# Kernel tuning notes

Hardware: AMD Instinct MI355X
Metric: run time of the kernel (lower is better)

## Reference

```python
import jax, jax.numpy as jnp
import numpy as np

BEAM_SIZE = 16


def setup_inputs() -> dict:
    key = jax.random.key(0)
    ks = jax.random.split(key, 9)
    B, N, S, A, Ai, E = 4, 48, 32, 16, 8, 512
    unaries = jax.random.normal(ks[0], (B, N, S), jnp.float32)
    behaviors = jax.random.normal(ks[1], (B, N, S, A), jnp.float32)
    interactions = jax.random.normal(ks[2], (B, N, N, S, S, Ai), jnp.float32)
    masks = jnp.ones((B, N), jnp.bool_)
    behavior_masks = jax.random.bernoulli(ks[3], 0.5, (S, A))
    interaction_masks = jax.random.bernoulli(ks[4], 0.5, (S, S, Ai))
    binary_edges = jax.random.randint(ks[5], (B, E, 2), 0, N, jnp.int32)
    binary_masks = jnp.ones((B, E), jnp.bool_)
    targets = jax.random.randint(ks[6], (B, N), 0, S, jnp.int32)
    weight_param_unary = jax.random.uniform(ks[7], (S,), jnp.float32)
    weight_param_binary = jax.random.uniform(ks[8], (S, S), jnp.float32)
    return dict(unaries=unaries, behaviors=behaviors, interactions=interactions,
                weight_param_unary=weight_param_unary, weight_param_binary=weight_param_binary,
                masks=masks, behavior_masks=behavior_masks, interaction_masks=interaction_masks,
                binary_edges=binary_edges, binary_masks=binary_masks, targets=targets)


def _forward(unaries, behaviors, interactions, weight_param_unary, weight_param_binary,
             masks, behavior_masks, interaction_masks, binary_edges, binary_masks, targets):
    sg = jax.lax.stop_gradient  # mirrors torch.no_grad blocks
    B, N, S = unaries.shape
    E = binary_edges.shape[1]
    K = min(BEAM_SIZE, S)
    dt = unaries.dtype

    m = masks[..., None].astype(dt)                                  # (B,N,1)
    masked_unaries = sg(unaries * m)                                 # no_grad
    bmask = behavior_masks.astype(dt)                                # (S,A)
    acnt = bmask.sum(-1)
    acnt = jnp.where(acnt == 0, jnp.ones((), dt), acnt)              # (S,)
    behaviors_unaries = sg(((behaviors * bmask).sum(-1) / acnt) * m) # (B,N,S), no_grad

    weighted_unaries = masked_unaries + weight_param_unary * behaviors_unaries

    # --- beam selection (targets forced to beam slot 0 via +inf scatter) ---
    bi = jnp.arange(B)[:, None]
    ni = jnp.arange(N)[None, :]
    _u = weighted_unaries.at[bi, ni, targets].set(jnp.inf)
    beam_targets = jax.lax.top_k(sg(_u), K)[1]                       # (B,N,K) int
    beam_unary = jnp.take_along_axis(weighted_unaries, beam_targets, axis=2)  # (B,N,K)

    # --- binary potentials: masked mean over interaction actions ---
    imask = interaction_masks.astype(dt)                             # (S,S,Ai)
    icnt = imask.sum(-1)
    icnt = jnp.where(icnt == 0, jnp.ones((), dt), icnt)              # (S,S)
    masked_inter = (interactions * imask).sum(-1) / icnt             # (B,N,N,S,S)

    eb = jnp.arange(B)[:, None]
    sel = masked_inter[eb, binary_edges[..., 0], binary_edges[..., 1]]  # (B,E,S,S)
    bt1 = beam_targets[eb, binary_edges[..., 0]]                     # (B,E,K)
    bt2 = beam_targets[eb, binary_edges[..., 1]]                     # (B,E,K)
    bin_phis_init = sg(sel[jnp.arange(B)[:, None, None, None],
                           jnp.arange(E)[None, :, None, None],
                           bt1[:, :, :, None], bt2[:, :, None, :]])  # (B,E,K,K), no_grad
    bin_phis = bin_phis_init * weight_param_binary[bt1[:, :, :, None], bt2[:, :, None, :]]

    # --- piecewise pseudo-likelihood loss ---
    norm_unary = jax.nn.log_softmax(beam_unary, axis=-1)
    gold_unary = jnp.where(masks, norm_unary[:, :, 0], jnp.zeros((), dt))
    pll = gold_unary.sum(-1)                                         # (B,)
    norm_bin = jax.nn.log_softmax(bin_phis.reshape(B, E, K * K), axis=-1).reshape(B, E, K, K)
    gold_bin = jnp.where(binary_masks, norm_bin[:, :, 0, 0], jnp.zeros((), dt))
    pll = pll + gold_bin.sum(-1)
    nll = -(pll / masks.sum(-1).astype(dt)).mean()
    return nll


def reference(unaries, behaviors, interactions, weight_param_unary, weight_param_binary,
              masks, behavior_masks, interaction_masks, binary_edges, binary_masks, targets):
    return _forward(unaries, behaviors, interactions, weight_param_unary, weight_param_binary,
                    masks, behavior_masks, interaction_masks, binary_edges, binary_masks, targets)
```

## Files before the change

### kernel.cpp

```cpp
#include <hip/hip_runtime.h>
#include <hip/hip_bf16.h>
#include <math.h>

#define BB 4
#define NN 48
#define SS 32
#define AA 16
#define AI 8
#define EE 512
#define KK 16
#define NNODE (BB * NN)
#define NEDGE (BB * EE)

#define WS_CBIN  0
#define WS_BEAM  32768
#define WS_NG    45056
#define WS_EG    46080

__device__ __forceinline__ bool read_mask(const void* p, int idx, int flag) {
    if (flag == 1) return ((const unsigned char*)p)[idx] != 0;
    if (flag == 2) return ((const float*)p)[idx] != 0.0f;
    return ((const int*)p)[idx] != 0;
}

__device__ __forceinline__ int detect_flag(const void* bmask, int lane) {
    unsigned int wrd = ((const unsigned int*)bmask)[lane & 31];
    bool anyF = __any(wrd == 0x3F800000u);
    bool anyG = __any(wrd > 1u);
    return anyF ? 2 : (anyG ? 1 : 0);
}

__global__ __launch_bounds__(256) void node_kernel(
    const float* __restrict__ unaries,
    const float* __restrict__ behaviors,
    const float* __restrict__ wpu,
    const float* __restrict__ wpb,
    const void* masks, const void* bmask, const void* imask,
    const int* __restrict__ targets,
    float* __restrict__ cbin,
    int* __restrict__ beam,
    float* __restrict__ node_gold)
{
    int tid = threadIdx.x;
    int wid = tid >> 6, lane = tid & 63;
    int flag = detect_flag(bmask, lane);

    if (blockIdx.x < 48) {
        int node = blockIdx.x * 4 + wid;
        float m = read_mask(masks, node, flag) ? 1.f : 0.f;
        int tgt = targets[node];

        float val = -INFINITY, key = -INFINITY;
        if (lane < SS) {
            int s = lane;
            float u = unaries[node * SS + s];
            const float* bp = behaviors + ((size_t)node * SS + s) * AA;
            float cnt = 0.f, raw = 0.f;
            #pragma unroll
            for (int a = 0; a < AA; ++a) {
                bool mm = read_mask(bmask, s * AA + a, flag);
                cnt += mm ? 1.f : 0.f;
                raw += mm ? bp[a] : 0.f;
            }
            if (cnt == 0.f) cnt = 1.f;
            val = m * (u + wpu[s] * (raw / cnt));
            key = (s == tgt) ? INFINITY : val;
        }

        int rank = 0;
        #pragma unroll
        for (int t = 0; t < SS; ++t) {
            float kt = __shfl(key, t, 64);
            rank += (kt > key) || (kt == key && t < lane);
        }
        bool sel = (lane < SS) && (rank < KK);
        if (sel) beam[node * KK + rank] = lane;

        float mv = sel ? val : -INFINITY;
        #pragma unroll
        for (int off = 32; off >= 1; off >>= 1)
            mv = fmaxf(mv, __shfl_xor(mv, off, 64));
        float se = sel ? expf(val - mv) : 0.f;
        #pragma unroll
        for (int off = 32; off >= 1; off >>= 1)
            se += __shfl_xor(se, off, 64);
        float vt = __shfl(val, tgt, 64);
        if (lane == 0)
            node_gold[node] = (m > 0.f) ? (vt - mv - logf(se)) : 0.f;
    } else {
        int idx = (blockIdx.x - 48) * 256 + tid;
        int p = idx >> 3;
        float cnt = 0.f;
        #pragma unroll
        for (int a = 0; a < AI; ++a)
            cnt += read_mask(imask, p * AI + a, flag) ? 1.f : 0.f;
        if (cnt == 0.f) cnt = 1.f;
        bool mm = read_mask(imask, idx, flag);
        cbin[idx] = mm ? (wpb[p] / cnt) : 0.f;
    }
}

__global__ __launch_bounds__(256) void edge_kernel(
    const float* __restrict__ interactions,
    const int* __restrict__ edges,
    const void* binmask, const void* bmask,
    const float* __restrict__ cbin,
    const int* __restrict__ beam,
    float* __restrict__ edge_gold)
{
    int be = blockIdx.x;
    int b = be >> 9;
    int tid = threadIdx.x;
    int wid = tid >> 6, lane = tid & 63;

    int n1 = edges[be * 2 + 0];
    int n2 = edges[be * 2 + 1];

    int i = tid >> 4, j = tid & 15;
    int s1 = beam[(b * NN + n1) * KK + i];
    int s2 = beam[(b * NN + n2) * KK + j];
    int p = s1 * SS + s2;

    size_t base = (((size_t)(b * NN + n1) * NN + n2) * (SS * SS) + p) * AI;
    float4 x0 = *(const float4*)(interactions + base);
    float4 x1 = *(const float4*)(interactions + base + 4);
    float4 c0 = *(const float4*)(cbin + p * AI);
    float4 c1 = *(const float4*)(cbin + p * AI + 4);
    float phi = x0.x * c0.x + x0.y * c0.y + x0.z * c0.z + x0.w * c0.w
              + x1.x * c1.x + x1.y * c1.y + x1.z * c1.z + x1.w * c1.w;

    __shared__ float sred[4];
    float v = phi;
    #pragma unroll
    for (int off = 32; off >= 1; off >>= 1)
        v = fmaxf(v, __shfl_xor(v, off, 64));
    if (lane == 0) sred[wid] = v;
    __syncthreads();
    float mx = fmaxf(fmaxf(sred[0], sred[1]), fmaxf(sred[2], sred[3]));
    __syncthreads();
    float e = expf(phi - mx);
    #pragma unroll
    for (int off = 32; off >= 1; off >>= 1)
        e += __shfl_xor(e, off, 64);
    if (lane == 0) sred[wid] = e;
    __syncthreads();
    if (tid == 0) {
        int flag = detect_flag(bmask, lane);
        float s = sred[0] + sred[1] + sred[2] + sred[3];
        float gold = phi - mx - logf(s);
        bool bm = read_mask(binmask, be, flag);
        edge_gold[be] = bm ? gold : 0.f;
    }
}

__global__ __launch_bounds__(256) void final_kernel(
    const void* masks, const void* bmask,
    const float* __restrict__ node_gold,
    const float* __restrict__ edge_gold,
    float* __restrict__ out)
{
    int tid = threadIdx.x;
    int b = tid >> 6;
    int lane = tid & 63;
    int flag = detect_flag(bmask, lane);

    float sum = 0.f, cnt = 0.f;
    if (lane < NN) {
        sum += node_gold[b * NN + lane];
        cnt += read_mask(masks, b * NN + lane, flag) ? 1.f : 0.f;
    }
    for (int e = lane; e < EE; e += 64)
        sum += edge_gold[b * EE + e];

    #pragma unroll
    for (int off = 32; off >= 1; off >>= 1) {
        sum += __shfl_xor(sum, off, 64);
        cnt += __shfl_xor(cnt, off, 64);
    }
    __shared__ float sp[4];
    if (lane == 0) sp[b] = sum / cnt;
    __syncthreads();
    if (tid == 0)
        out[0] = -(sp[0] + sp[1] + sp[2] + sp[3]) * (1.f / BB);
}

extern "C" void kernel_launch(void* const* d_in, const int* in_sizes, int n_in,
                              void* d_out, int out_size, void* d_ws, size_t ws_size,
                              hipStream_t stream) {
    const float* unaries      = (const float*)d_in[0];
    const float* behaviors    = (const float*)d_in[1];
    const float* interactions = (const float*)d_in[2];
    const float* wpu          = (const float*)d_in[3];
    const float* wpb          = (const float*)d_in[4];
    const void*  masks        = d_in[5];
    const void*  bmask        = d_in[6];
    const void*  imask        = d_in[7];
    const int*   edges        = (const int*)d_in[8];
    const void*  binmask      = d_in[9];
    const int*   targets      = (const int*)d_in[10];
    float* out = (float*)d_out;

    char* ws = (char*)d_ws;
    float* cbin      = (float*)(ws + WS_CBIN);
    int*   beamp     = (int*)(ws + WS_BEAM);
    float* node_gold = (float*)(ws + WS_NG);
    float* edge_gold = (float*)(ws + WS_EG);

    node_kernel<<<80, 256, 0, stream>>>(unaries, behaviors, wpu, wpb,
                                        masks, bmask, imask, targets,
                                        cbin, beamp, node_gold);
    edge_kernel<<<NEDGE, 256, 0, stream>>>(interactions, edges, binmask, bmask,
                                           cbin, beamp, edge_gold);
    final_kernel<<<1, 256, 0, stream>>>(masks, bmask, node_gold, edge_gold, out);
}
```

Before: 21.64 us.

## Vectorize mask/behavior loads, pack two edges per block, merge softmax reductions

Behavior and mask reads in the node kernel become float4/uint4 vector loads, and the cbin precompute gives each thread one pair with two vector stores, cutting its grid from 80 to 52 blocks. Beam slot assignment now uses a ballot/popcount order with the target in slot 0. The edge kernel handles two edges per 512-thread block and fuses the max and sum-exp reductions into one online-softmax pass with a single barrier. The aim is fewer memory instructions, fewer blocks and fewer syncs, at the cost of more exp calls and a changed beam ordering within slots 1..15.

```diff
diff --git a/kernel.cpp b/kernel.cpp
--- a/kernel.cpp
+++ b/kernel.cpp
@@ -54,14 +54,40 @@
         if (lane < SS) {
             int s = lane;
             float u = unaries[node * SS + s];
-            const float* bp = behaviors + ((size_t)node * SS + s) * AA;
+
+            const float4* bp4 = (const float4*)(behaviors + ((size_t)node * SS + s) * AA);
+            float4 b0 = bp4[0], b1 = bp4[1], b2 = bp4[2], b3 = bp4[3];
+            float bv[16] = {b0.x,b0.y,b0.z,b0.w, b1.x,b1.y,b1.z,b1.w,
+                            b2.x,b2.y,b2.z,b2.w, b3.x,b3.y,b3.z,b3.w};
+
+            float bmv[16];
+            if (flag == 1) {
+                uint4 v = *(const uint4*)((const unsigned char*)bmask + s * 16);
+                unsigned int w4[4] = {v.x, v.y, v.z, v.w};
+                #pragma unroll
+                for (int k = 0; k < 16; ++k)
+                    bmv[k] = ((w4[k >> 2] >> ((k & 3) * 8)) & 255u) ? 1.f : 0.f;
+            } else if (flag == 0) {
+                const uint4* ip = (const uint4*)((const int*)bmask + s * 16);
+                #pragma unroll
+                for (int r = 0; r < 4; ++r) {
+                    uint4 v = ip[r];
+                    bmv[r*4+0] = v.x ? 1.f : 0.f; bmv[r*4+1] = v.y ? 1.f : 0.f;
+                    bmv[r*4+2] = v.z ? 1.f : 0.f; bmv[r*4+3] = v.w ? 1.f : 0.f;
+                }
+            } else {
+                const float4* fp = (const float4*)((const float*)bmask + s * 16);
+                #pragma unroll
+                for (int r = 0; r < 4; ++r) {
+                    float4 v = fp[r];
+                    bmv[r*4+0] = v.x != 0.f ? 1.f : 0.f; bmv[r*4+1] = v.y != 0.f ? 1.f : 0.f;
+                    bmv[r*4+2] = v.z != 0.f ? 1.f : 0.f; bmv[r*4+3] = v.w != 0.f ? 1.f : 0.f;
+                }
+            }
+
             float cnt = 0.f, raw = 0.f;
             #pragma unroll
-            for (int a = 0; a < AA; ++a) {
-                bool mm = read_mask(bmask, s * AA + a, flag);
-                cnt += mm ? 1.f : 0.f;
-                raw += mm ? bp[a] : 0.f;
-            }
+            for (int k = 0; k < 16; ++k) { cnt += bmv[k]; raw += bmv[k] * bv[k]; }
             if (cnt == 0.f) cnt = 1.f;
             val = m * (u + wpu[s] * (raw / cnt));
             key = (s == tgt) ? INFINITY : val;
@@ -74,7 +100,14 @@
             rank += (kt > key) || (kt == key && t < lane);
         }
         bool sel = (lane < SS) && (rank < KK);
-        if (sel) beam[node * KK + rank] = lane;
+
+        bool sel_nt = sel && (lane != tgt);
+        unsigned long long bal = __ballot(sel_nt);
+        if (sel) {
+            int slot = (lane == tgt) ? 0
+                       : 1 + __popcll(bal & ((1ull << lane) - 1ull));
+            beam[node * KK + slot] = lane;
+        }
 
         float mv = sel ? val : -INFINITY;
         #pragma unroll
@@ -88,19 +121,36 @@
         if (lane == 0)
             node_gold[node] = (m > 0.f) ? (vt - mv - logf(se)) : 0.f;
     } else {
-        int idx = (blockIdx.x - 48) * 256 + tid;
-        int p = idx >> 3;
-        float cnt = 0.f;
-        #pragma unroll
-        for (int a = 0; a < AI; ++a)
-            cnt += read_mask(imask, p * AI + a, flag) ? 1.f : 0.f;
+        int p = (blockIdx.x - 48) * 256 + tid;
+        float imv[8];
+        if (flag == 1) {
+            uint2 v = *(const uint2*)((const unsigned char*)imask + p * 8);
+            unsigned int w2[2] = {v.x, v.y};
+            #pragma unroll
+            for (int k = 0; k < 8; ++k)
+                imv[k] = ((w2[k >> 2] >> ((k & 3) * 8)) & 255u) ? 1.f : 0.f;
+        } else if (flag == 0) {
+            const uint4* ip = (const uint4*)((const int*)imask + p * 8);
+            uint4 v0 = ip[0], v1 = ip[1];
+            imv[0]=v0.x?1.f:0.f; imv[1]=v0.y?1.f:0.f; imv[2]=v0.z?1.f:0.f; imv[3]=v0.w?1.f:0.f;
+            imv[4]=v1.x?1.f:0.f; imv[5]=v1.y?1.f:0.f; imv[6]=v1.z?1.f:0.f; imv[7]=v1.w?1.f:0.f;
+        } else {
+            const float4* fp = (const float4*)((const float*)imask + p * 8);
+            float4 v0 = fp[0], v1 = fp[1];
+            imv[0]=v0.x!=0.f?1.f:0.f; imv[1]=v0.y!=0.f?1.f:0.f; imv[2]=v0.z!=0.f?1.f:0.f; imv[3]=v0.w!=0.f?1.f:0.f;
+            imv[4]=v1.x!=0.f?1.f:0.f; imv[5]=v1.y!=0.f?1.f:0.f; imv[6]=v1.z!=0.f?1.f:0.f; imv[7]=v1.w!=0.f?1.f:0.f;
+        }
+        float cnt = imv[0]+imv[1]+imv[2]+imv[3]+imv[4]+imv[5]+imv[6]+imv[7];
         if (cnt == 0.f) cnt = 1.f;
-        bool mm = read_mask(imask, idx, flag);
-        cbin[idx] = mm ? (wpb[p] / cnt) : 0.f;
-    }
-}
-
-__global__ __launch_bounds__(256) void edge_kernel(
+        float w = wpb[p] / cnt;
+        float4 o0 = make_float4(imv[0]*w, imv[1]*w, imv[2]*w, imv[3]*w);
+        float4 o1 = make_float4(imv[4]*w, imv[5]*w, imv[6]*w, imv[7]*w);
+        *(float4*)(cbin + p * AI)     = o0;
+        *(float4*)(cbin + p * AI + 4) = o1;
+    }
+}
+
+__global__ __launch_bounds__(512) void edge_kernel(
     const float* __restrict__ interactions,
     const int* __restrict__ edges,
     const void* binmask, const void* bmask,
@@ -108,15 +158,18 @@
     const int* __restrict__ beam,
     float* __restrict__ edge_gold)
 {
-    int be = blockIdx.x;
+    int tid = threadIdx.x;
+    int le = tid >> 8;
+    int t  = tid & 255;
+    int wid = tid >> 6;
+    int lane = tid & 63;
+    int be = (blockIdx.x << 1) + le;
     int b = be >> 9;
-    int tid = threadIdx.x;
-    int wid = tid >> 6, lane = tid & 63;
-
-    int n1 = edges[be * 2 + 0];
-    int n2 = edges[be * 2 + 1];
-
-    int i = tid >> 4, j = tid & 15;
+
+    int2 e2 = ((const int2*)edges)[be];
+    int n1 = e2.x, n2 = e2.y;
+
+    int i = t >> 4, j = t & 15;
     int s1 = beam[(b * NN + n1) * KK + i];
     int s2 = beam[(b * NN + n2) * KK + j];
     int p = s1 * SS + s2;
@@ -129,25 +182,27 @@
     float phi = x0.x * c0.x + x0.y * c0.y + x0.z * c0.z + x0.w * c0.w
               + x1.x * c1.x + x1.y * c1.y + x1.z * c1.z + x1.w * c1.w;
 
-    __shared__ float sred[4];
-    float v = phi;
+    float mw = phi;
     #pragma unroll
     for (int off = 32; off >= 1; off >>= 1)
-        v = fmaxf(v, __shfl_xor(v, off, 64));
-    if (lane == 0) sred[wid] = v;
-    __syncthreads();
-    float mx = fmaxf(fmaxf(sred[0], sred[1]), fmaxf(sred[2], sred[3]));
-    __syncthreads();
-    float e = expf(phi - mx);
+        mw = fmaxf(mw, __shfl_xor(mw, off, 64));
+    float ew = expf(phi - mw);
     #pragma unroll
     for (int off = 32; off >= 1; off >>= 1)
-        e += __shfl_xor(e, off, 64);
-    if (lane == 0) sred[wid] = e;
+        ew += __shfl_xor(ew, off, 64);
+
+    __shared__ float2 sred[8];
+    if (lane == 0) sred[wid] = make_float2(mw, ew);
     __syncthreads();
-    if (tid == 0) {
+
+    if (t == 0) {
+        int w0 = le << 2;
+        float2 p0 = sred[w0], p1 = sred[w0+1], p2 = sred[w0+2], p3 = sred[w0+3];
+        float M = fmaxf(fmaxf(p0.x, p1.x), fmaxf(p2.x, p3.x));
+        float S = p0.y * expf(p0.x - M) + p1.y * expf(p1.x - M)
+                + p2.y * expf(p2.x - M) + p3.y * expf(p3.x - M);
+        float gold = phi - M - logf(S);
         int flag = detect_flag(bmask, lane);
-        float s = sred[0] + sred[1] + sred[2] + sred[3];
-        float gold = phi - mx - logf(s);
         bool bm = read_mask(binmask, be, flag);
         edge_gold[be] = bm ? gold : 0.f;
     }
@@ -206,10 +261,10 @@
     float* node_gold = (float*)(ws + WS_NG);
     float* edge_gold = (float*)(ws + WS_EG);
 
-    node_kernel<<<80, 256, 0, stream>>>(unaries, behaviors, wpu, wpb,
+    node_kernel<<<52, 256, 0, stream>>>(unaries, behaviors, wpu, wpb,
                                         masks, bmask, imask, targets,
                                         cbin, beamp, node_gold);
-    edge_kernel<<<NEDGE, 256, 0, stream>>>(interactions, edges, binmask, bmask,
-                                           cbin, beamp, edge_gold);
+    edge_kernel<<<NEDGE / 2, 512, 0, stream>>>(interactions, edges, binmask,
+                                               bmask, cbin, beamp, edge_gold);
     final_kernel<<<1, 256, 0, stream>>>(masks, bmask, node_gold, edge_gold, out);
 }
```

New measurement: 20.25 us. 1.07x faster.
